# Kernel tuning notes

Measured on AMD Instinct MI355X. Metric: run time of the kernel, lower is better.

## Reference

```python
import jax, jax.numpy as jnp
import numpy as np


def gcn_conv(x, edge_index, W, b):
    """PyG-style GCNConv: add self loops, symmetric normalization, sum-aggregate."""
    N = x.shape[0]
    loop = jnp.arange(N, dtype=edge_index.dtype)
    src = jnp.concatenate([edge_index[0], loop])
    dst = jnp.concatenate([edge_index[1], loop])
    # degree computed on target (col) index with unit edge weights
    deg = jax.ops.segment_sum(jnp.ones_like(dst, dtype=x.dtype), dst, num_segments=N)
    dinv = jnp.where(deg > 0, jax.lax.rsqrt(deg), 0.0)
    norm = dinv[src] * dinv[dst]            # [E+N]
    h = x @ W                               # [N, out]
    msg = h[src] * norm[:, None]            # gather + scale
    out = jax.ops.segment_sum(msg, dst, num_segments=N)  # scatter-add
    return out + b


def global_mean_pool(x, batch, num_graphs):
    s = jax.ops.segment_sum(x, batch, num_segments=num_graphs)
    cnt = jax.ops.segment_sum(jnp.ones((x.shape[0],), x.dtype), batch, num_segments=num_graphs)
    return s / jnp.maximum(cnt, 1.0)[:, None]


NUM_GRAPHS = 64


def setup_inputs() -> dict:
    key = jax.random.key(0)
    ks = jax.random.split(key, 20)
    N, E = 100000, 1600000
    inp = {
        "x_origin": jax.random.normal(ks[0], (N, 25), jnp.float32),
        "edge_index_origin": jax.random.randint(ks[1], (2, E), 0, N, jnp.int64),
        "batch_origin": jnp.sort(jax.random.randint(ks[2], (N,), 0, NUM_GRAPHS, jnp.int64)),
        "x_line": jax.random.normal(ks[3], (N, 51), jnp.float32),
        "edge_index_line": jax.random.randint(ks[4], (2, E), 0, N, jnp.int64),
        "batch_line": jnp.sort(jax.random.randint(ks[5], (N,), 0, NUM_GRAPHS, jnp.int64)),
        # learned params (Glorot-ish scale)
        "W1": jax.random.normal(ks[6], (25, 128), jnp.float32) * 0.1,
        "b1": jnp.zeros((128,), jnp.float32),
        "W2": jax.random.normal(ks[7], (128, 64), jnp.float32) * 0.08,
        "b2": jnp.zeros((64,), jnp.float32),
        "W5": jax.random.normal(ks[8], (64, 5), jnp.float32) * 0.1,
        "b5": jnp.zeros((5,), jnp.float32),
        "W3": jax.random.normal(ks[9], (51, 64), jnp.float32) * 0.1,
        "b3": jnp.zeros((64,), jnp.float32),
        "W4": jax.random.normal(ks[10], (64, 5), jnp.float32) * 0.1,
        "b4": jnp.zeros((5,), jnp.float32),
        "Wfc": jax.random.normal(ks[11], (10, 2), jnp.float32) * 0.2,
        "bfc": jnp.zeros((2,), jnp.float32),
    }
    return inp


def reference(x_origin, edge_index_origin, batch_origin,
              x_line, edge_index_line, batch_line,
              W1, b1, W2, b2, W5, b5, W3, b3, W4, b4, Wfc, bfc):
    # origin branch
    h = jax.nn.relu(gcn_conv(x_origin, edge_index_origin, W1, b1))
    h = jax.nn.relu(gcn_conv(h, edge_index_origin, W2, b2))
    h = gcn_conv(h, edge_index_origin, W5, b5)
    g_origin = global_mean_pool(h, batch_origin, NUM_GRAPHS)  # [G, 5]
    # line branch
    hl = jax.nn.relu(gcn_conv(x_line, edge_index_line, W3, b3))
    hl = gcn_conv(hl, edge_index_line, W4, b4)
    g_line = global_mean_pool(hl, batch_line, NUM_GRAPHS)     # [G, 5]
    x = jnp.concatenate([g_origin, g_line], axis=1) @ Wfc + bfc  # [G, 2]
    return jax.nn.log_softmax(x, axis=1)
```

## Files before the change

### kernel.cpp

```cpp
#include <hip/hip_runtime.h>
#include <math.h>

#define NUM_G 64
#define CAP 32
#define SL 128
#define CHUNK_Q 1024
#define SEGCAP 32
#define MAXR 800
#define MAXNBA 1024
#define LSTR 33
#define ABLK 512

typedef unsigned short u16;
typedef unsigned int u32;
typedef int vint4 __attribute__((ext_vector_type(4)));
typedef short bf16x8 __attribute__((ext_vector_type(8)));
typedef float f32x4 __attribute__((ext_vector_type(4)));

__device__ inline u16 f2bf(float f) {
    u32 u = __float_as_uint(f);
    u32 r = u + 0x7FFF + ((u >> 16) & 1);
    return (u16)(r >> 16);
}
__device__ inline float bf2f(u16 h) { return __uint_as_float((u32)h << 16); }
__device__ inline float bflo(u32 p) { return __uint_as_float(p << 16); }
__device__ inline float bfhi(u32 p) { return __uint_as_float(p & 0xFFFF0000u); }

__device__ inline int slice_of(int d, float pinv) {
    int s = (int)((float)d * pinv);
    return s > SL - 1 ? SL - 1 : s;
}


__global__ void k_bin(const int* __restrict__ ei_o, const int* __restrict__ ei_l,
                      u32* __restrict__ binbuf, int* __restrict__ cntbuf,
                      int E, int NBA, float pinv) {
    __shared__ int lcnt[2 * SL];
    for (int i = threadIdx.x; i < 2 * SL; i += 256) lcnt[i] = 0;
    __syncthreads();
    const int qE = E >> 2;
    const int TQ = 2 * qE;
    const int b = blockIdx.x;
    for (int k = 0; k < CHUNK_Q; k += 256) {
        int qi = b * CHUNK_Q + k + threadIdx.x;
        if (qi >= TQ) break;
        int g = qi >= qE;
        int e4 = (g ? qi - qE : qi) * 4;
        const int* ei = g ? ei_l : ei_o;
        vint4 d4 = __builtin_nontemporal_load((const vint4*)(ei + E + e4));
        vint4 s4 = __builtin_nontemporal_load((const vint4*)(ei + e4));
        #pragma unroll
        for (int j = 0; j < 4; j++) {
            int d = d4[j];
            int bin = g * SL + slice_of(d, pinv);
            int rank = atomicAdd(&lcnt[bin], 1);
            if (rank < SEGCAP) {
                u32 pk = ((u32)(d & 1023) << 17) | (u32)s4[j];
                binbuf[((size_t)(bin * NBA + b)) * SEGCAP + rank] = pk;
            }
        }
    }
    __syncthreads();
    for (int i = threadIdx.x; i < 2 * SL; i += 256)
        cntbuf[i * NBA + b] = min(lcnt[i], SEGCAP);
}

__global__ __launch_bounds__(ABLK, 1)
void k_assemble(const u32* __restrict__ binbuf, const int* __restrict__ cntbuf,
                const int* __restrict__ ei_o, const int* __restrict__ ei_l,
                int* __restrict__ adj_o, int* __restrict__ adj_l,
                int* __restrict__ deg_o, int* __restrict__ deg_l,
                float* __restrict__ dinv_o, float* __restrict__ dinv_l,
                int N, int E, int NBA, float pinv) {
    const int g = blockIdx.x >> 7;
    const int s = blockIdx.x & (SL - 1);

    int lo, hi;
    { int a = 0, b2 = N; while (a < b2) { int m = (a + b2) >> 1;
        if (slice_of(m, pinv) >= s) b2 = m; else a = m + 1; } lo = a; }
    { int a = lo, b2 = N; while (a < b2) { int m = (a + b2) >> 1;
        if (slice_of(m, pinv) >= s + 1) b2 = m; else a = m + 1; } hi = a; }
    const int R = hi - lo;

    __shared__ int ladj[MAXR * LSTR];
    __shared__ int cnt[MAXR];
    __shared__ int segcnt[MAXNBA];
    for (int i = threadIdx.x; i < R; i += ABLK) cnt[i] = 0;
    const int bin = g * SL + s;
    for (int i = threadIdx.x; i < NBA; i += ABLK) segcnt[i] = cntbuf[bin * NBA + i];
    __syncthreads();

    const u32* base = binbuf + (size_t)bin * NBA * SEGCAP;
    const int total = NBA * SEGCAP;
    const int lo10 = lo & 1023;
    for (int i = threadIdx.x; i < total; i += ABLK) {
        int seg = i >> 5;
        int idx = i & (SEGCAP - 1);
        if (idx >= segcnt[seg]) continue;
        u32 pk = __builtin_nontemporal_load(base + i);
        int drel = ((int)(pk >> 17) - lo10) & 1023;
        int src = (int)(pk & 0x1FFFFu);
        int r = atomicAdd(&cnt[drel], 1);
        if (r < CAP) ladj[drel * LSTR + r] = src;
    }
    int tbase = (E >> 2) * 4, rem = E - tbase;
    if (threadIdx.x < rem) {
        const int* ei = g ? ei_l : ei_o;
        int e = tbase + threadIdx.x;
        int d = ei[E + e];
        if (d >= lo && d < hi) {
            int r = atomicAdd(&cnt[d - lo], 1);
            if (r < CAP) ladj[(d - lo) * LSTR + r] = ei[e];
        }
    }
    __syncthreads();

    for (int r = threadIdx.x; r < R; r += ABLK) {
        int c = min(cnt[r], CAP);
        int* row = &ladj[r * LSTR];
        int v[CAP];
        #pragma unroll
        for (int a = 0; a < CAP; a++) v[a] = (a < c) ? row[a] : 0x7FFFFFFF;
        #pragma unroll
        for (int k = 2; k <= CAP; k <<= 1) {
            #pragma unroll
            for (int j = k >> 1; j > 0; j >>= 1) {
                #pragma unroll
                for (int i = 0; i < CAP; i++) {
                    int ixj = i ^ j;
                    if (ixj > i) {
                        bool up = ((i & k) == 0);
                        int a = v[i], b = v[ixj];
                        bool sw = up ? (a > b) : (a < b);
                        v[i] = sw ? b : a;
                        v[ixj] = sw ? a : b;
                    }
                }
            }
        }
        #pragma unroll
        for (int a = 0; a < CAP; a++) row[a] = v[a];
    }
    __syncthreads();

    int* adj = g ? adj_l : adj_o;
    int* deg = g ? deg_l : deg_o;
    float* dinv = g ? dinv_l : dinv_o;
    for (int i = threadIdx.x; i < R * CAP; i += ABLK) {
        int r = i >> 5, c = i & 31;
        adj[(size_t)lo * CAP + i] = ladj[r * LSTR + c];
    }
    for (int i = threadIdx.x; i < R; i += ABLK) {
        int c = cnt[i];
        deg[lo + i] = c;
        dinv[lo + i] = rsqrtf((float)(c + 1));
    }
}


__global__ void k_prep(const float* __restrict__ xo, const float* __restrict__ xl,
                       const float* __restrict__ dinv_o, const float* __restrict__ dinv_l,
                       u16* __restrict__ Xpo, u16* __restrict__ Xpl, int N) {
    int idx = blockIdx.x * 256 + threadIdx.x;
    int t1 = N * 32;
    if (idx < t1) {
        int v = idx >> 5, c = idx & 31;
        float val = (c < 25) ? xo[(size_t)v * 25 + c] * dinv_o[v] : 0.f;
        Xpo[idx] = f2bf(val);
    } else {
        int j = idx - t1;
        if (j < N * 64) {
            int v = j >> 6, c = j & 63;
            float val = (c < 51) ? xl[(size_t)v * 51 + c] * dinv_l[v] : 0.f;
            Xpl[j] = f2bf(val);
        }
    }
}

template <int K, int F, int MODE>
__global__ __launch_bounds__(256)
void k_gemm_mfma_t(const u16* __restrict__ X, const float* __restrict__ W,
                   const float* __restrict__ sb, u16* __restrict__ S, int N, int Kreal) {
    const int KP = K + 8;
    __shared__ u16 Wt[F * KP];
    for (int i = threadIdx.x; i < Kreal * F; i += 256) {
        int k = i / F, n = i % F;
        Wt[n * KP + k] = f2bf(W[i]);
    }
    for (int i = threadIdx.x; i < (K - Kreal) * F; i += 256) {
        int k = Kreal + i / F, n = i % F;
        Wt[n * KP + k] = 0;
    }
    __syncthreads();

    const int wave = threadIdx.x >> 6;
    const int lane = threadIdx.x & 63;
    const int m = lane & 15;
    const int kgrp = lane >> 4;
    const int row0 = blockIdx.x * 64 + wave * 16;
    const int arow = row0 + m;
    const bool ok = arow < N;

    bf16x8 afrag[K / 32];
    const u16* xr = X + (size_t)arow * K;
    #pragma unroll
    for (int kc = 0; kc < K / 32; kc++) {
        if (ok) afrag[kc] = *(const bf16x8*)(xr + kc * 32 + kgrp * 8);
        else    afrag[kc] = bf16x8{0, 0, 0, 0, 0, 0, 0, 0};
    }

    #pragma unroll
    for (int nt = 0; nt < F / 16; nt++) {
        f32x4 acc = f32x4{0.f, 0.f, 0.f, 0.f};
        #pragma unroll
        for (int kc = 0; kc < K / 32; kc++) {
            bf16x8 bfrag = *(const bf16x8*)(&Wt[(nt * 16 + m) * KP + kc * 32 + kgrp * 8]);
            acc = __builtin_amdgcn_mfma_f32_16x16x32_bf16(afrag[kc], bfrag, acc, 0, 0, 0);
        }
        #pragma unroll
        for (int r = 0; r < 4; r++) {
            int orow = row0 + kgrp * 4 + r;
            if (orow < N) {
                float o;
                if (MODE == 0) o = acc[r] * sb[orow];
                else { o = acc[r] + sb[nt * 16 + m]; o = fmaxf(o, 0.f); }
                S[(size_t)orow * F + nt * 16 + m] = f2bf(o);
            }
        }
    }
}

__global__ void k_gemm_small(const u16* __restrict__ X, const float* __restrict__ W,
                             const float* __restrict__ dinv, float* __restrict__ S,
                             int N, int K, int F) {
    __shared__ float Ws[1024];
    int KF = K * F;
    for (int i = threadIdx.x; i < KF; i += blockDim.x) Ws[i] = W[i];
    __syncthreads();
    int idx = blockIdx.x * blockDim.x + threadIdx.x;
    if (idx >= N * F) return;
    int row = idx / F;
    int col = idx - row * F;
    const u16* xr = X + (size_t)row * K;
    float acc = 0.f;
    for (int k = 0; k < K; k++) acc = fmaf(bf2f(xr[k]), Ws[k * F + col], acc);
    S[idx] = acc * dinv[row];
}

__global__ void k_agg8(const u16* __restrict__ S, const int* __restrict__ deg,
                       const int* __restrict__ adj, const float* __restrict__ dinv,
                       const float* __restrict__ bias, u16* __restrict__ Y,
                       int N, int F8, int relu) {
    int idx = blockIdx.x * blockDim.x + threadIdx.x;
    if (idx >= N * F8) return;
    int v = idx / F8;
    int f8 = idx - v * F8;
    const uint4* Sq = (const uint4*)S;

    uint4 p = Sq[(size_t)v * F8 + f8];
    float a0 = bflo(p.x), a1 = bfhi(p.x), a2 = bflo(p.y), a3 = bfhi(p.y);
    float a4 = bflo(p.z), a5 = bfhi(p.z), a6 = bflo(p.w), a7 = bfhi(p.w);

    int dg = min(deg[v], CAP);
    const int* av = adj + v * CAP;
    int i = 0;
    for (; i + 4 <= dg; i += 4) {
        vint4 u4 = *(const vint4*)(av + i);
        uint4 q0 = Sq[(size_t)u4.x * F8 + f8];
        uint4 q1 = Sq[(size_t)u4.y * F8 + f8];
        uint4 q2 = Sq[(size_t)u4.z * F8 + f8];
        uint4 q3 = Sq[(size_t)u4.w * F8 + f8];
        a0 += bflo(q0.x); a1 += bfhi(q0.x); a2 += bflo(q0.y); a3 += bfhi(q0.y);
        a4 += bflo(q0.z); a5 += bfhi(q0.z); a6 += bflo(q0.w); a7 += bfhi(q0.w);
        a0 += bflo(q1.x); a1 += bfhi(q1.x); a2 += bflo(q1.y); a3 += bfhi(q1.y);
        a4 += bflo(q1.z); a5 += bfhi(q1.z); a6 += bflo(q1.w); a7 += bfhi(q1.w);
        a0 += bflo(q2.x); a1 += bfhi(q2.x); a2 += bflo(q2.y); a3 += bfhi(q2.y);
        a4 += bflo(q2.z); a5 += bfhi(q2.z); a6 += bflo(q2.w); a7 += bfhi(q2.w);
        a0 += bflo(q3.x); a1 += bfhi(q3.x); a2 += bflo(q3.y); a3 += bfhi(q3.y);
        a4 += bflo(q3.z); a5 += bfhi(q3.z); a6 += bflo(q3.w); a7 += bfhi(q3.w);
    }
    for (; i < dg; i++) {
        int u = av[i];
        uint4 q = Sq[(size_t)u * F8 + f8];
        a0 += bflo(q.x); a1 += bfhi(q.x);
        a2 += bflo(q.y); a3 += bfhi(q.y);
        a4 += bflo(q.z); a5 += bfhi(q.z);
        a6 += bflo(q.w); a7 += bfhi(q.w);
    }
    float dv = dinv[v];
    const float* bp = bias + 8 * f8;
    float o[8] = {dv*a0 + bp[0], dv*a1 + bp[1], dv*a2 + bp[2], dv*a3 + bp[3],
                  dv*a4 + bp[4], dv*a5 + bp[5], dv*a6 + bp[6], dv*a7 + bp[7]};
    if (relu) {
        #pragma unroll
        for (int j = 0; j < 8; j++) o[j] = fmaxf(o[j], 0.f);
    }
    uint4 pk;
    pk.x = (u32)f2bf(o[0]) | ((u32)f2bf(o[1]) << 16);
    pk.y = (u32)f2bf(o[2]) | ((u32)f2bf(o[3]) << 16);
    pk.z = (u32)f2bf(o[4]) | ((u32)f2bf(o[5]) << 16);
    pk.w = (u32)f2bf(o[6]) | ((u32)f2bf(o[7]) << 16);
    *(uint4*)(Y + (size_t)v * (F8 * 8) + f8 * 8) = pk;
}

__global__ void k_agg5_pool(const float* __restrict__ S, const int* __restrict__ deg,
                            const int* __restrict__ adj, const float* __restrict__ dinv,
                            const float* __restrict__ bias, const int* __restrict__ batch,
                            float* __restrict__ gsum, float* __restrict__ gcnt, int N) {
    __shared__ float sacc[NUM_G * 5];
    __shared__ float scnt[NUM_G];
    for (int i = threadIdx.x; i < NUM_G * 5; i += blockDim.x) sacc[i] = 0.f;
    for (int i = threadIdx.x; i < NUM_G; i += blockDim.x) scnt[i] = 0.f;
    __syncthreads();
    int v = blockIdx.x * blockDim.x + threadIdx.x;
    if (v < N) {
        const float* sv = S + v * 5;
        float a0 = sv[0], a1 = sv[1], a2 = sv[2], a3 = sv[3], a4 = sv[4];
        int dg = min(deg[v], CAP);
        const int* av = adj + v * CAP;
        int i = 0;
        for (; i + 2 <= dg; i += 2) {
            int ua = av[i], ub = av[i + 1];
            const float* pa = S + ua * 5;
            const float* pb = S + ub * 5;
            float b0 = pa[0], b1 = pa[1], b2 = pa[2], b3 = pa[3], b4 = pa[4];
            float c0 = pb[0], c1 = pb[1], c2 = pb[2], c3 = pb[3], c4 = pb[4];
            a0 += b0 + c0; a1 += b1 + c1; a2 += b2 + c2; a3 += b3 + c3; a4 += b4 + c4;
        }
        for (; i < dg; i++) {
            const float* p = S + av[i] * 5;
            a0 += p[0]; a1 += p[1]; a2 += p[2]; a3 += p[3]; a4 += p[4];
        }
        float dv = dinv[v];
        int b = batch[v];
        atomicAdd(&sacc[b * 5 + 0], dv * a0 + bias[0]);
        atomicAdd(&sacc[b * 5 + 1], dv * a1 + bias[1]);
        atomicAdd(&sacc[b * 5 + 2], dv * a2 + bias[2]);
        atomicAdd(&sacc[b * 5 + 3], dv * a3 + bias[3]);
        atomicAdd(&sacc[b * 5 + 4], dv * a4 + bias[4]);
        atomicAdd(&scnt[b], 1.f);
    }
    __syncthreads();
    for (int i = threadIdx.x; i < NUM_G * 5; i += blockDim.x)
        if (sacc[i] != 0.f) atomicAdd(&gsum[i], sacc[i]);
    for (int i = threadIdx.x; i < NUM_G; i += blockDim.x)
        if (scnt[i] != 0.f) atomicAdd(&gcnt[i], scnt[i]);
}

__global__ void k_head(const float* __restrict__ gsum_o, const float* __restrict__ gcnt_o,
                       const float* __restrict__ gsum_l, const float* __restrict__ gcnt_l,
                       const float* __restrict__ Wfc, const float* __restrict__ bfc,
                       float* __restrict__ out, int G) {
    int g = threadIdx.x;
    if (g >= G) return;
    float feat[10];
    float co = fmaxf(gcnt_o[g], 1.f);
    float cl = fmaxf(gcnt_l[g], 1.f);
    for (int f = 0; f < 5; f++) feat[f]     = gsum_o[g * 5 + f] / co;
    for (int f = 0; f < 5; f++) feat[5 + f] = gsum_l[g * 5 + f] / cl;
    float z0 = bfc[0], z1 = bfc[1];
    for (int i = 0; i < 10; i++) {
        z0 += feat[i] * Wfc[i * 2 + 0];
        z1 += feat[i] * Wfc[i * 2 + 1];
    }
    float m = fmaxf(z0, z1);
    float lse = m + logf(expf(z0 - m) + expf(z1 - m));
    out[g * 2 + 0] = z0 - lse;
    out[g * 2 + 1] = z1 - lse;
}


extern "C" void kernel_launch(void* const* d_in, const int* in_sizes, int n_in,
                              void* d_out, int out_size, void* d_ws, size_t ws_size,
                              hipStream_t stream) {
    const float* x_o   = (const float*)d_in[0];
    const int*   ei_o  = (const int*)d_in[1];
    const int*   bat_o = (const int*)d_in[2];
    const float* x_l   = (const float*)d_in[3];
    const int*   ei_l  = (const int*)d_in[4];
    const int*   bat_l = (const int*)d_in[5];
    const float* W1  = (const float*)d_in[6];   const float* b1  = (const float*)d_in[7];
    const float* W2  = (const float*)d_in[8];   const float* b2  = (const float*)d_in[9];
    const float* W5  = (const float*)d_in[10];  const float* b5  = (const float*)d_in[11];
    const float* W3  = (const float*)d_in[12];  const float* b3  = (const float*)d_in[13];
    const float* W4  = (const float*)d_in[14];  const float* b4  = (const float*)d_in[15];
    const float* Wfc = (const float*)d_in[16];  const float* bfc = (const float*)d_in[17];
    float* out = (float*)d_out;

    const int N = in_sizes[0] / 25;
    const int E = in_sizes[1] / 2;
    const int G = NUM_G;

    int nb = (N + 255) / 256;
    int nb64 = (N + 63) / 64;
    int TQ = 2 * (E >> 2);
    int NBA = (TQ + CHUNK_Q - 1) / CHUNK_Q;

    float* gsum_o = (float*)d_ws;
    float* gsum_l = gsum_o + G * 5;
    float* gcnt_o = gsum_l + G * 5;
    float* gcnt_l = gcnt_o + G;
    float* zb     = gcnt_l + G;
    int* deg_o = (int*)(zb + 64);
    int* deg_l = deg_o + N;
    float* dinv_o = (float*)(deg_l + N);
    float* dinv_l = dinv_o + N;
    int* cntbuf = (int*)(dinv_l + N);
    int* adj_o = cntbuf + 2 * SL * NBA;
    int* adj_l = adj_o + (size_t)N * CAP;
    u16* bufS = (u16*)(adj_l + (size_t)N * CAP);
    u16* bufY = bufS + (size_t)N * 128;
    u16* Xpo  = bufY + (size_t)N * 128;
    u16* Xpl  = Xpo + (size_t)N * 32;
    u32* binbuf = (u32*)bufS;

    size_t zero_bytes = (size_t)(2 * G * 5 + 2 * G + 64) * sizeof(float);
    hipMemsetAsync(d_ws, 0, zero_bytes, stream);

    float pinv = (float)SL / (float)N;
    k_bin<<<NBA, 256, 0, stream>>>(ei_o, ei_l, binbuf, cntbuf, E, NBA, pinv);
    k_assemble<<<2 * SL, ABLK, 0, stream>>>(binbuf, cntbuf, ei_o, ei_l,
                                            adj_o, adj_l, deg_o, deg_l,
                                            dinv_o, dinv_l, N, E, NBA, pinv);
    k_prep<<<(N * 96 + 255) / 256, 256, 0, stream>>>(x_o, x_l, dinv_o, dinv_l, Xpo, Xpl, N);

    k_agg8<<<(N * 4 + 255) / 256, 256, 0, stream>>>(Xpo, deg_o, adj_o, dinv_o, zb, bufY, N, 4, 0);
    k_gemm_mfma_t<32, 128, 1><<<nb64, 256, 0, stream>>>(bufY, W1, b1, bufS, N, 25);
    k_gemm_mfma_t<128, 64, 0><<<nb64, 256, 0, stream>>>(bufS, W2, dinv_o, bufY, N, 128);
    k_agg8<<<(N * 8 + 255) / 256, 256, 0, stream>>>(bufY, deg_o, adj_o, dinv_o, b2, bufS, N, 8, 1);
    k_gemm_small<<<(N * 5 + 255) / 256, 256, 0, stream>>>(bufS, W5, dinv_o, (float*)bufY, N, 64, 5);
    k_agg5_pool<<<nb, 256, 0, stream>>>((float*)bufY, deg_o, adj_o, dinv_o, b5, bat_o, gsum_o, gcnt_o, N);

    k_agg8<<<(N * 8 + 255) / 256, 256, 0, stream>>>(Xpl, deg_l, adj_l, dinv_l, zb, bufS, N, 8, 0);
    k_gemm_mfma_t<64, 64, 1><<<nb64, 256, 0, stream>>>(bufS, W3, b3, bufY, N, 51);
    k_gemm_small<<<(N * 5 + 255) / 256, 256, 0, stream>>>(bufY, W4, dinv_l, (float*)bufS, N, 64, 5);
    k_agg5_pool<<<nb, 256, 0, stream>>>((float*)bufS, deg_l, adj_l, dinv_l, b4, bat_l, gsum_l, gcnt_l, N);

    k_head<<<1, 64, 0, stream>>>(gsum_o, gcnt_o, gsum_l, gcnt_l, Wfc, bfc, out, G);
}
```

Before: 362.8 us.

## Fuse origin and line branches into shared launches and fold prep into assemble

Folds the feature-prep pass (dinv scaling and bf16 packing) into the adjacency assemble kernel, using a shared-memory copy of dinv. Pairs independent origin- and line-branch stages into combined launches that select their work by block index: pre-aggregation, first GEMMs, second GEMM with the small GEMM, and aggregation with pooling. Buffers are reassigned so the two branches can live side by side. The small GEMM also gains vectorized 8-wide bf16 loads. The aim is fewer launches and better device fill for small per-stage grids. The cost is more complex buffer aliasing and heterogeneous blocks sharing shared-memory sizing.

```diff
diff --git a/kernel.cpp b/kernel.cpp
--- a/kernel.cpp
+++ b/kernel.cpp
@@ -71,6 +71,8 @@
                 int* __restrict__ adj_o, int* __restrict__ adj_l,
                 int* __restrict__ deg_o, int* __restrict__ deg_l,
                 float* __restrict__ dinv_o, float* __restrict__ dinv_l,
+                const float* __restrict__ x_o, const float* __restrict__ x_l,
+                u16* __restrict__ Xpo, u16* __restrict__ Xpl,
                 int N, int E, int NBA, float pinv) {
     const int g = blockIdx.x >> 7;
     const int s = blockIdx.x & (SL - 1);
@@ -85,6 +87,7 @@
     __shared__ int ladj[MAXR * LSTR];
     __shared__ int cnt[MAXR];
     __shared__ int segcnt[MAXNBA];
+    __shared__ float sdinv[MAXR];
     for (int i = threadIdx.x; i < R; i += ABLK) cnt[i] = 0;
     const int bin = g * SL + s;
     for (int i = threadIdx.x; i < NBA; i += ABLK) segcnt[i] = cntbuf[bin * NBA + i];
@@ -153,36 +156,30 @@
     for (int i = threadIdx.x; i < R; i += ABLK) {
         int c = cnt[i];
         deg[lo + i] = c;
-        dinv[lo + i] = rsqrtf((float)(c + 1));
-    }
-}
-
-
-__global__ void k_prep(const float* __restrict__ xo, const float* __restrict__ xl,
-                       const float* __restrict__ dinv_o, const float* __restrict__ dinv_l,
-                       u16* __restrict__ Xpo, u16* __restrict__ Xpl, int N) {
-    int idx = blockIdx.x * 256 + threadIdx.x;
-    int t1 = N * 32;
-    if (idx < t1) {
-        int v = idx >> 5, c = idx & 31;
-        float val = (c < 25) ? xo[(size_t)v * 25 + c] * dinv_o[v] : 0.f;
-        Xpo[idx] = f2bf(val);
-    } else {
-        int j = idx - t1;
-        if (j < N * 64) {
-            int v = j >> 6, c = j & 63;
-            float val = (c < 51) ? xl[(size_t)v * 51 + c] * dinv_l[v] : 0.f;
-            Xpl[j] = f2bf(val);
-        }
-    }
-}
+        float dv = rsqrtf((float)(c + 1));
+        dinv[lo + i] = dv;
+        sdinv[i] = dv;
+    }
+    __syncthreads();
+
+    const float* xsrc = g ? x_l : x_o;
+    u16* Xp = g ? Xpl : Xpo;
+    const int FR = g ? 51 : 25;
+    const int SH = g ? 6 : 5;
+    const int FC = 1 << SH;
+    for (int i = threadIdx.x; i < (R << SH); i += ABLK) {
+        int r = i >> SH, c = i & (FC - 1);
+        float val = (c < FR) ? xsrc[(size_t)(lo + r) * FR + c] * sdinv[r] : 0.f;
+        Xp[((size_t)(lo + r) << SH) + c] = f2bf(val);
+    }
+}
+
 
 template <int K, int F, int MODE>
-__global__ __launch_bounds__(256)
-void k_gemm_mfma_t(const u16* __restrict__ X, const float* __restrict__ W,
-                   const float* __restrict__ sb, u16* __restrict__ S, int N, int Kreal) {
+__device__ void gemm_body(u16* Wt, int bidx, const u16* __restrict__ X,
+                          const float* __restrict__ W, const float* __restrict__ sb,
+                          u16* __restrict__ S, int N, int Kreal) {
     const int KP = K + 8;
-    __shared__ u16 Wt[F * KP];
     for (int i = threadIdx.x; i < Kreal * F; i += 256) {
         int k = i / F, n = i % F;
         Wt[n * KP + k] = f2bf(W[i]);
@@ -197,7 +194,7 @@
     const int lane = threadIdx.x & 63;
     const int m = lane & 15;
     const int kgrp = lane >> 4;
-    const int row0 = blockIdx.x * 64 + wave * 16;
+    const int row0 = bidx * 64 + wave * 16;
     const int arow = row0 + m;
     const bool ok = arow < N;
 
@@ -230,28 +227,38 @@
     }
 }
 
-__global__ void k_gemm_small(const u16* __restrict__ X, const float* __restrict__ W,
-                             const float* __restrict__ dinv, float* __restrict__ S,
-                             int N, int K, int F) {
-    __shared__ float Ws[1024];
+__device__ void small_body(float* Ws, int bidx, const u16* __restrict__ X,
+                           const float* __restrict__ W, const float* __restrict__ dinv,
+                           float* __restrict__ S, int N, int K, int F) {
     int KF = K * F;
-    for (int i = threadIdx.x; i < KF; i += blockDim.x) Ws[i] = W[i];
-    __syncthreads();
-    int idx = blockIdx.x * blockDim.x + threadIdx.x;
+    for (int i = threadIdx.x; i < KF; i += 256) Ws[i] = W[i];
+    __syncthreads();
+    int idx = bidx * 256 + threadIdx.x;
     if (idx >= N * F) return;
     int row = idx / F;
     int col = idx - row * F;
-    const u16* xr = X + (size_t)row * K;
+    const uint4* xq = (const uint4*)(X + (size_t)row * K);
     float acc = 0.f;
-    for (int k = 0; k < K; k++) acc = fmaf(bf2f(xr[k]), Ws[k * F + col], acc);
+    for (int k8 = 0; k8 < K / 8; k8++) {
+        uint4 p = xq[k8];
+        const float* wk = Ws + (k8 * 8) * F + col;
+        acc = fmaf(bflo(p.x), wk[0 * F], acc);
+        acc = fmaf(bfhi(p.x), wk[1 * F], acc);
+        acc = fmaf(bflo(p.y), wk[2 * F], acc);
+        acc = fmaf(bfhi(p.y), wk[3 * F], acc);
+        acc = fmaf(bflo(p.z), wk[4 * F], acc);
+        acc = fmaf(bfhi(p.z), wk[5 * F], acc);
+        acc = fmaf(bflo(p.w), wk[6 * F], acc);
+        acc = fmaf(bfhi(p.w), wk[7 * F], acc);
+    }
     S[idx] = acc * dinv[row];
 }
 
-__global__ void k_agg8(const u16* __restrict__ S, const int* __restrict__ deg,
-                       const int* __restrict__ adj, const float* __restrict__ dinv,
-                       const float* __restrict__ bias, u16* __restrict__ Y,
-                       int N, int F8, int relu) {
-    int idx = blockIdx.x * blockDim.x + threadIdx.x;
+__device__ void agg8_body(int bidx, const u16* __restrict__ S, const int* __restrict__ deg,
+                          const int* __restrict__ adj, const float* __restrict__ dinv,
+                          const float* __restrict__ bias, u16* __restrict__ Y,
+                          int N, int F8, int relu) {
+    int idx = bidx * 256 + threadIdx.x;
     if (idx >= N * F8) return;
     int v = idx / F8;
     int f8 = idx - v * F8;
@@ -303,16 +310,16 @@
     *(uint4*)(Y + (size_t)v * (F8 * 8) + f8 * 8) = pk;
 }
 
-__global__ void k_agg5_pool(const float* __restrict__ S, const int* __restrict__ deg,
-                            const int* __restrict__ adj, const float* __restrict__ dinv,
-                            const float* __restrict__ bias, const int* __restrict__ batch,
-                            float* __restrict__ gsum, float* __restrict__ gcnt, int N) {
+__device__ void agg5_pool_body(int bidx, const float* __restrict__ S, const int* __restrict__ deg,
+                               const int* __restrict__ adj, const float* __restrict__ dinv,
+                               const float* __restrict__ bias, const int* __restrict__ batch,
+                               float* __restrict__ gsum, float* __restrict__ gcnt, int N) {
     __shared__ float sacc[NUM_G * 5];
     __shared__ float scnt[NUM_G];
-    for (int i = threadIdx.x; i < NUM_G * 5; i += blockDim.x) sacc[i] = 0.f;
-    for (int i = threadIdx.x; i < NUM_G; i += blockDim.x) scnt[i] = 0.f;
-    __syncthreads();
-    int v = blockIdx.x * blockDim.x + threadIdx.x;
+    for (int i = threadIdx.x; i < NUM_G * 5; i += 256) sacc[i] = 0.f;
+    for (int i = threadIdx.x; i < NUM_G; i += 256) scnt[i] = 0.f;
+    __syncthreads();
+    int v = bidx * 256 + threadIdx.x;
     if (v < N) {
         const float* sv = S + v * 5;
         float a0 = sv[0], a1 = sv[1], a2 = sv[2], a3 = sv[3], a4 = sv[4];
@@ -341,10 +348,71 @@
         atomicAdd(&scnt[b], 1.f);
     }
     __syncthreads();
-    for (int i = threadIdx.x; i < NUM_G * 5; i += blockDim.x)
+    for (int i = threadIdx.x; i < NUM_G * 5; i += 256)
         if (sacc[i] != 0.f) atomicAdd(&gsum[i], sacc[i]);
-    for (int i = threadIdx.x; i < NUM_G; i += blockDim.x)
+    for (int i = threadIdx.x; i < NUM_G; i += 256)
         if (scnt[i] != 0.f) atomicAdd(&gcnt[i], scnt[i]);
+}
+
+
+__global__ __launch_bounds__(256)
+void k_preagg_both(const u16* Xpo, const int* deg_o, const int* adj_o,
+                   const float* dinv_o, const float* zb, u16* Ao,
+                   const u16* Xpl, const int* deg_l, const int* adj_l,
+                   const float* dinv_l, u16* Al, int N, int nbA) {
+    if ((int)blockIdx.x < nbA)
+        agg8_body(blockIdx.x, Xpo, deg_o, adj_o, dinv_o, zb, Ao, N, 4, 0);
+    else
+        agg8_body(blockIdx.x - nbA, Xpl, deg_l, adj_l, dinv_l, zb, Al, N, 8, 0);
+}
+
+__global__ __launch_bounds__(256)
+void k_gemm1_both(const u16* Ao, const float* W1, const float* b1, u16* H1,
+                  const u16* Al, const float* W3, const float* b3, u16* HL1,
+                  int N, int nbA) {
+    __shared__ u16 Wt[5120];
+    if ((int)blockIdx.x < nbA)
+        gemm_body<32, 128, 1>(Wt, blockIdx.x, Ao, W1, b1, H1, N, 25);
+    else
+        gemm_body<64, 64, 1>(Wt, blockIdx.x - nbA, Al, W3, b3, HL1, N, 51);
+}
+
+__global__ __launch_bounds__(256)
+void k_gemm2_both(const u16* H1, const float* W2, const float* dinv_o, u16* S2,
+                  const u16* HL1, const float* W4, const float* dinv_l, float* S5l,
+                  int N, int nbA) {
+    __shared__ float smem[4352];
+    if ((int)blockIdx.x < nbA)
+        gemm_body<128, 64, 0>((u16*)smem, blockIdx.x, H1, W2, dinv_o, S2, N, 128);
+    else
+        small_body(smem, blockIdx.x - nbA, HL1, W4, dinv_l, S5l, N, 64, 5);
+}
+
+__global__ __launch_bounds__(256)
+void k_aggpool_both(const u16* S2, const int* deg_o, const int* adj_o,
+                    const float* dinv_o, const float* b2, u16* H2,
+                    const float* S5l, const int* deg_l, const int* adj_l,
+                    const float* dinv_l, const float* b4, const int* bat_l,
+                    float* gsum_l, float* gcnt_l, int N, int nbA) {
+    if ((int)blockIdx.x < nbA)
+        agg8_body(blockIdx.x, S2, deg_o, adj_o, dinv_o, b2, H2, N, 8, 1);
+    else
+        agg5_pool_body(blockIdx.x - nbA, S5l, deg_l, adj_l, dinv_l, b4, bat_l,
+                       gsum_l, gcnt_l, N);
+}
+
+__global__ __launch_bounds__(256)
+void k_gemm_small(const u16* X, const float* W, const float* dinv,
+                  float* S, int N, int K, int F) {
+    __shared__ float Ws[512];
+    small_body(Ws, blockIdx.x, X, W, dinv, S, N, K, F);
+}
+
+__global__ __launch_bounds__(256)
+void k_agg5_pool(const float* S, const int* deg, const int* adj, const float* dinv,
+                 const float* bias, const int* batch,
+                 float* gsum, float* gcnt, int N) {
+    agg5_pool_body(blockIdx.x, S, deg, adj, dinv, bias, batch, gsum, gcnt, N);
 }
 
 __global__ void k_head(const float* __restrict__ gsum_o, const float* __restrict__ gcnt_o,
@@ -408,11 +476,20 @@
     int* cntbuf = (int*)(dinv_l + N);
     int* adj_o = cntbuf + 2 * SL * NBA;
     int* adj_l = adj_o + (size_t)N * CAP;
-    u16* bufS = (u16*)(adj_l + (size_t)N * CAP);
-    u16* bufY = bufS + (size_t)N * 128;
-    u16* Xpo  = bufY + (size_t)N * 128;
+    u16* bufA = (u16*)(adj_l + (size_t)N * CAP);
+    u16* bufB = bufA + (size_t)N * 128;
+    u16* Xpo  = bufB + (size_t)N * 128;
     u16* Xpl  = Xpo + (size_t)N * 32;
-    u32* binbuf = (u32*)bufS;
+
+    u32* binbuf = (u32*)bufA;
+    u16* Ao  = bufB;
+    u16* Al  = bufB + (size_t)N * 32;
+    u16* H1  = bufA;
+    u16* HL1 = Xpl;
+    u16* S2  = bufB;
+    float* S5l = (float*)(bufB + (size_t)N * 64);
+    u16* H2  = bufA;
+    float* S5o = (float*)Xpo;
 
     size_t zero_bytes = (size_t)(2 * G * 5 + 2 * G + 64) * sizeof(float);
     hipMemsetAsync(d_ws, 0, zero_bytes, stream);
@@ -421,20 +498,24 @@
     k_bin<<<NBA, 256, 0, stream>>>(ei_o, ei_l, binbuf, cntbuf, E, NBA, pinv);
     k_assemble<<<2 * SL, ABLK, 0, stream>>>(binbuf, cntbuf, ei_o, ei_l,
                                             adj_o, adj_l, deg_o, deg_l,
-                                            dinv_o, dinv_l, N, E, NBA, pinv);
-    k_prep<<<(N * 96 + 255) / 256, 256, 0, stream>>>(x_o, x_l, dinv_o, dinv_l, Xpo, Xpl, N);
-
-    k_agg8<<<(N * 4 + 255) / 256, 256, 0, stream>>>(Xpo, deg_o, adj_o, dinv_o, zb, bufY, N, 4, 0);
-    k_gemm_mfma_t<32, 128, 1><<<nb64, 256, 0, stream>>>(bufY, W1, b1, bufS, N, 25);
-    k_gemm_mfma_t<128, 64, 0><<<nb64, 256, 0, stream>>>(bufS, W2, dinv_o, bufY, N, 128);
-    k_agg8<<<(N * 8 + 255) / 256, 256, 0, stream>>>(bufY, deg_o, adj_o, dinv_o, b2, bufS, N, 8, 1);
-    k_gemm_small<<<(N * 5 + 255) / 256, 256, 0, stream>>>(bufS, W5, dinv_o, (float*)bufY, N, 64, 5);
-    k_agg5_pool<<<nb, 256, 0, stream>>>((float*)bufY, deg_o, adj_o, dinv_o, b5, bat_o, gsum_o, gcnt_o, N);
-
-    k_agg8<<<(N * 8 + 255) / 256, 256, 0, stream>>>(Xpl, deg_l, adj_l, dinv_l, zb, bufS, N, 8, 0);
-    k_gemm_mfma_t<64, 64, 1><<<nb64, 256, 0, stream>>>(bufS, W3, b3, bufY, N, 51);
-    k_gemm_small<<<(N * 5 + 255) / 256, 256, 0, stream>>>(bufY, W4, dinv_l, (float*)bufS, N, 64, 5);
-    k_agg5_pool<<<nb, 256, 0, stream>>>((float*)bufS, deg_l, adj_l, dinv_l, b4, bat_l, gsum_l, gcnt_l, N);
-
+                                            dinv_o, dinv_l, x_o, x_l, Xpo, Xpl,
+                                            N, E, NBA, pinv);
+
+    int nb_pA = (N * 4 + 255) / 256;
+    int nb_pB = (N * 8 + 255) / 256;
+    k_preagg_both<<<nb_pA + nb_pB, 256, 0, stream>>>(Xpo, deg_o, adj_o, dinv_o, zb, Ao,
+                                                     Xpl, deg_l, adj_l, dinv_l, Al,
+                                                     N, nb_pA);
+    k_gemm1_both<<<2 * nb64, 256, 0, stream>>>(Ao, W1, b1, H1, Al, W3, b3, HL1, N, nb64);
+    int nb_sL = (N * 5 + 255) / 256;
+    k_gemm2_both<<<nb64 + nb_sL, 256, 0, stream>>>(H1, W2, dinv_o, S2,
+                                                   HL1, W4, dinv_l, S5l, N, nb64);
+    int nb_a = (N * 8 + 255) / 256;
+    k_aggpool_both<<<nb_a + nb, 256, 0, stream>>>(S2, deg_o, adj_o, dinv_o, b2, H2,
+                                                  S5l, deg_l, adj_l, dinv_l, b4, bat_l,
+                                                  gsum_l, gcnt_l, N, nb_a);
+    k_gemm_small<<<nb_sL, 256, 0, stream>>>(H2, W5, dinv_o, S5o, N, 64, 5);
+    k_agg5_pool<<<nb, 256, 0, stream>>>(S5o, deg_o, adj_o, dinv_o, b5, bat_o,
+                                        gsum_o, gcnt_o, N);
     k_head<<<1, 64, 0, stream>>>(gsum_o, gcnt_o, gsum_l, gcnt_l, Wfc, bfc, out, G);
 }
```

Result: slower. 401.2 us (+10.6%).
